# Kernel tuning notes

Hardware: AMD Instinct MI355X
Metric: run time of the kernel (lower is better)

Reference implementation:

```python
import jax, jax.numpy as jnp
import numpy as np

B, T, D, DFF, E = 4, 2048, 1024, 4096, 8


def setup_inputs() -> dict:
    key = jax.random.key(0)
    ks = jax.random.split(key, 4)
    s_in = 1.0 / np.sqrt(D)
    s_ff = 1.0 / np.sqrt(DFF)
    return {
        "x": jax.random.normal(ks[0], (B, T, D), dtype=jnp.float32),
        "gate_W": jax.random.normal(ks[1], (D, E), dtype=jnp.float32) * s_in,
        "gate_b": jnp.zeros((E,), dtype=jnp.float32),
        "W1": jax.random.normal(ks[2], (E, D, DFF), dtype=jnp.float32) * s_in,
        "b1": jnp.zeros((E, DFF), dtype=jnp.float32),
        "W2": jax.random.normal(ks[3], (E, DFF, D), dtype=jnp.float32) * s_ff,
        "b2": jnp.zeros((E, D), dtype=jnp.float32),
    }


def reference(x, gate_W, gate_b, W1, b1, W2, b2):
    # x: [B, T, D]. Top-1 gated MoE; each expert FFN runs on the (masked)
    # full token set, exactly as the original dense-masked implementation.
    b, t, d = x.shape
    num_experts = gate_W.shape[-1]
    logits = jnp.einsum("btd,de->bte", x, gate_W) + gate_b  # [B,T,E]
    top1 = jnp.argmax(logits, axis=-1).reshape(-1)          # [B*T]
    flat_x = x.reshape(b * t, d)                            # [N,D]
    out = jnp.zeros_like(flat_x)
    for e in range(num_experts):  # small fixed expert count
        mask = (top1 == e).astype(x.dtype)[:, None]         # [N,1]
        h = jax.nn.gelu((flat_x * mask) @ W1[e] + b1[e], approximate=False)
        out = out + (h @ W2[e] + b2[e]) * mask
    return out.reshape(b, t, d)
```

## Files before the change

kernel.cpp:

```cpp
#include <hip/hip_runtime.h>
#include <hip/hip_bf16.h>
#include <cstdint>

#define N_TOK 8192
#define D_IN  1024
#define DFF   4096
#define NE    8
#define DEPTH 3
#define MAXT256 40

typedef __bf16 bf16x8 __attribute__((ext_vector_type(8)));
typedef float  f32x4  __attribute__((ext_vector_type(4)));

__device__ __forceinline__ unsigned short f2bf(float f) {
  unsigned u = __float_as_uint(f);
  u += 0x7fffu + ((u >> 16) & 1u);
  return (unsigned short)(u >> 16);
}

__device__ __forceinline__ void gll16(const void* g, void* l) {
  __builtin_amdgcn_global_load_lds(
      (__attribute__((address_space(1))) void*)g,
      (__attribute__((address_space(3))) void*)l, 16, 0, 0);
}

__global__ __launch_bounds__(256) void gate_kernel(
    const float* __restrict__ x, const float* __restrict__ gW,
    const float* __restrict__ gb, unsigned short* __restrict__ xbf,
    int* __restrict__ top1) {
  int wave = threadIdx.x >> 6, lane = threadIdx.x & 63;
  int n = blockIdx.x * 4 + wave;
  const float* xr = x + (size_t)n * D_IN;
  double acc[NE];
#pragma unroll
  for (int e = 0; e < NE; ++e) acc[e] = 0.0;
#pragma unroll
  for (int j = 0; j < 16; ++j) {
    int d = j * 64 + lane;
    float v = xr[d];
    xbf[(size_t)n * D_IN + d] = f2bf(v);
    float4 g0 = *(const float4*)(gW + (size_t)d * 8);
    float4 g1 = *(const float4*)(gW + (size_t)d * 8 + 4);
    acc[0] += (double)v * (double)g0.x;
    acc[1] += (double)v * (double)g0.y;
    acc[2] += (double)v * (double)g0.z;
    acc[3] += (double)v * (double)g0.w;
    acc[4] += (double)v * (double)g1.x;
    acc[5] += (double)v * (double)g1.y;
    acc[6] += (double)v * (double)g1.z;
    acc[7] += (double)v * (double)g1.w;
  }
#pragma unroll
  for (int m = 32; m >= 1; m >>= 1) {
#pragma unroll
    for (int e = 0; e < NE; ++e) acc[e] += __shfl_xor(acc[e], m);
  }
  if (lane == 0) {
    float best = (float)acc[0] + gb[0];
    int be = 0;
#pragma unroll
    for (int e = 1; e < NE; ++e) {
      float lv = (float)acc[e] + gb[e];
      if (lv > best) { best = lv; be = e; }
    }
    top1[n] = be;
  }
}

__global__ __launch_bounds__(1024) void build_kernel(
    const int* __restrict__ top1, int* __restrict__ hdr, int* __restrict__ perm,
    int* __restrict__ tile_e, int* __restrict__ tile_m, int* __restrict__ sub0,
    int* __restrict__ t256_e, int* __restrict__ t256_m, int* __restrict__ t256_s) {
  __shared__ int cnt[NE];
  int tid = threadIdx.x;
  if (tid < NE) cnt[tid] = 0;
  __syncthreads();
  int mye[8], myp[8];
#pragma unroll
  for (int r = 0; r < 8; ++r) {
    int n = r * 1024 + tid;
    int e = top1[n];
    mye[r] = e;
    myp[r] = atomicAdd(&cnt[e], 1);
  }
  __syncthreads();
  if (tid == 0) {
    int o = 0;
    int n1 = 0, n2 = 0, n256 = 0;
    for (int e = 0; e < NE; ++e) {
      int Me = cnt[e];
      hdr[e] = Me;
      hdr[8 + e] = o;
      o += Me;
    }
    hdr[16] = o;
    for (int e = 0; e < NE; ++e) {
      int Me = cnt[e];
      int base2 = n2;
      n2 += (Me + 63) >> 6;
      for (int m0 = 0; m0 < Me; m0 += 128) {
        tile_e[n1] = e; tile_m[n1] = m0; sub0[n1] = base2 + (m0 >> 6); ++n1;
      }
      for (int m0 = 0; m0 < Me; m0 += 256) {
        t256_e[n256] = e; t256_m[n256] = m0; t256_s[n256] = base2 + (m0 >> 6); ++n256;
      }
    }
    hdr[17] = n1;
    hdr[18] = n2;
    hdr[19] = n256;
  }
  __syncthreads();
#pragma unroll
  for (int r = 0; r < 8; ++r) {
    int n = r * 1024 + tid;
    perm[mye[r] * N_TOK + myp[r]] = n;
  }
}

__global__ __launch_bounds__(256) void apack256_kernel(
    const unsigned short* __restrict__ xbf, const int* __restrict__ hdr,
    const int* __restrict__ t256_e, const int* __restrict__ t256_m,
    const int* __restrict__ perm, unsigned short* __restrict__ Apack) {
  int ti = blockIdx.x >> 3;
  if (ti >= hdr[19]) return;
  int part = blockIdx.x & 7;
  int h = part >> 2, ktq = part & 3;
  int e = t256_e[ti], m0 = t256_m[ti], Me = hdr[e];
  int w = threadIdx.x >> 6, lane = threadIdx.x & 63;
  int kq = lane >> 4, m = lane & 15;
#pragma unroll
  for (int g2 = 0; g2 < 2; ++g2) {
    int g = w * 2 + g2;
    int r = m0 + h * 128 + g * 16 + m;
    if (r >= Me) r = Me - 1;
    int token = perm[e * N_TOK + r];
    const char* src = (const char*)xbf + (size_t)token * 2048 + kq * 16;
    char* dst = (char*)Apack + (size_t)ti * 524288 + h * 8192 + g * 1024 + lane * 16;
#pragma unroll
    for (int kt2 = 0; kt2 < 8; ++kt2) {
      int kt = ktq * 8 + kt2;
      *(int4*)(dst + (size_t)kt * 16384) = *(const int4*)(src + kt * 64);
    }
  }
}

__device__ __forceinline__ void wpack_w1_body(
    const float* __restrict__ src, unsigned short* __restrict__ dst, int bid) {
  __shared__ unsigned short tile[64][72];
  int e = bid >> 10;
  int t = bid & 1023;
  int r0 = (t >> 6) * 64, c0 = (t & 63) * 64;
  const float* s = src + (size_t)e * D_IN * DFF;
  int tr = threadIdx.x >> 4, tc = (threadIdx.x & 15) * 4;
#pragma unroll
  for (int p = 0; p < 4; ++p) {
    int row = r0 + tr + p * 16;
    const float4 v = *(const float4*)(s + (size_t)row * DFF + c0 + tc);
    tile[tc + 0][tr + p * 16] = f2bf(v.x);
    tile[tc + 1][tr + p * 16] = f2bf(v.y);
    tile[tc + 2][tr + p * 16] = f2bf(v.z);
    tile[tc + 3][tr + p * 16] = f2bf(v.w);
  }
  __syncthreads();
#pragma unroll
  for (int u = 0; u < 2; ++u) {
    int c = u * 256 + threadIdx.x;
    int kk_l = c >> 8, gg_l = (c >> 6) & 3, kq = (c >> 4) & 3, mm = c & 15;
    int fl = gg_l * 16 + mm;
    int kl = kk_l * 32 + kq * 8;
    int4 val = *(const int4*)&tile[fl][kl];
    int f = c0 + fl;
    int nt = f >> 8, h = (f >> 7) & 1, g = (f >> 4) & 7;
    int kt = (r0 >> 5) + kk_l;
    size_t off = ((size_t)(e * 16 + nt) * 32 + kt) * 16384 +
                 (size_t)h * 8192 + g * 1024 + (kq * 16 + mm) * 16;
    *(int4*)((char*)dst + off) = val;
  }
}

__device__ __forceinline__ void wpack_body(
    const float* __restrict__ src, unsigned short* __restrict__ dst,
    int R, int C, int tiles_r, int tiles_c, int bid) {
  __shared__ unsigned short tile[64][72];
  int tpe = tiles_r * tiles_c;
  int e = bid / tpe;
  int t = bid % tpe;
  int r0 = (t / tiles_c) * 64, c0 = (t % tiles_c) * 64;
  const float* s = src + (size_t)e * R * C;
  int tr = threadIdx.x >> 4, tc = (threadIdx.x & 15) * 4;
#pragma unroll
  for (int p = 0; p < 4; ++p) {
    int row = r0 + tr + p * 16;
    const float4 v = *(const float4*)(s + (size_t)row * C + c0 + tc);
    tile[tc + 0][tr + p * 16] = f2bf(v.x);
    tile[tc + 1][tr + p * 16] = f2bf(v.y);
    tile[tc + 2][tr + p * 16] = f2bf(v.z);
    tile[tc + 3][tr + p * 16] = f2bf(v.w);
  }
  __syncthreads();
  int nkk = R >> 5, ntc = C >> 7;
#pragma unroll
  for (int u = 0; u < 2; ++u) {
    int c = u * 256 + threadIdx.x;
    int kk_l = c >> 8, gg_l = (c >> 6) & 3, kq = (c >> 4) & 3, mm = c & 15;
    int fl = gg_l * 16 + mm;
    int kl = kk_l * 32 + kq * 8;
    int4 val = *(const int4*)&tile[fl][kl];
    int f = c0 + fl;
    int nt = f >> 7, gg = (f >> 4) & 7;
    int kk = (r0 >> 5) + kk_l;
    size_t off = ((((size_t)e * ntc + nt) * nkk + kk) * 8 + gg) * 1024 + (kq * 16 + mm) * 16;
    *(int4*)((char*)dst + off) = val;
  }
}

__global__ __launch_bounds__(256) void wpack_both(
    const float* __restrict__ W1, unsigned short* __restrict__ B1,
    const float* __restrict__ W2, unsigned short* __restrict__ B2) {
  if (blockIdx.x < NE * 16 * 64)
    wpack_w1_body(W1, B1, blockIdx.x);
  else
    wpack_body(W2, B2, DFF, D_IN, 64, 16, blockIdx.x - NE * 16 * 64);
}

__global__ __launch_bounds__(512, 2) void gemm1_256(
    const unsigned short* __restrict__ Apack, const unsigned short* __restrict__ Bpack1,
    const float* __restrict__ b1, const int* __restrict__ hdr,
    const int* __restrict__ t256_e, const int* __restrict__ t256_m,
    const int* __restrict__ t256_s, unsigned short* __restrict__ Hpack) {
  int ti = blockIdx.x >> 4;
  if (ti >= hdr[19]) return;
  int nt = blockIdx.x & 15;
  int e = t256_e[ti], m0 = t256_m[ti], Me = hdr[e];
  int n0 = nt * 256;

  extern __shared__ __align__(16) char smem[];

  int tid = threadIdx.x, wave = tid >> 6, lane = tid & 63;
  int wm = wave >> 2, wn = wave & 3;

  const char* aBase = (const char*)Apack + (size_t)ti * 524288;
  const char* bBase = (const char*)Bpack1 + (size_t)(e * 16 + nt) * 524288;

  auto stage = [&](int kt) {
    int b = kt % 3;
    const char* sB = bBase + (size_t)kt * 16384 + tid * 16;
    char* dB = smem + 49152 + b * 16384 + tid * 16;
    gll16(sB, dB);
    gll16(sB + 8192, dB + 8192);
    const char* sA = aBase + (size_t)kt * 16384 + tid * 16;
    char* dA = smem + b * 16384 + tid * 16;
    gll16(sA, dA);
    gll16(sA + 8192, dA + 8192);
  };

  stage(0);
  stage(1);

  f32x4 acc[8][4];
#pragma unroll
  for (int i = 0; i < 8; ++i)
#pragma unroll
    for (int j = 0; j < 4; ++j) { f32x4 z = {0.f, 0.f, 0.f, 0.f}; acc[i][j] = z; }

  const int NITER = D_IN / 32;
  for (int T = 0; T < NITER; ++T) {
    asm volatile("s_waitcnt vmcnt(4)" ::: "memory");
    __builtin_amdgcn_s_barrier();
    int nx = T + 2;
    if (nx > NITER - 1) nx = NITER - 1;
    stage(nx);
    int b = T % 3;
    const char* Ap = smem + b * 16384 + wm * 8192 + lane * 16;
    const char* Bp = smem + 49152 + b * 16384 + (wn >> 1) * 8192 + (wn & 1) * 4096 + lane * 16;
    bf16x8 a[8], bf[4];
#pragma unroll
    for (int i = 0; i < 8; ++i) a[i] = *(const bf16x8*)(Ap + i * 1024);
#pragma unroll
    for (int j = 0; j < 4; ++j) bf[j] = *(const bf16x8*)(Bp + j * 1024);
#pragma unroll
    for (int i = 0; i < 8; ++i)
#pragma unroll
      for (int j = 0; j < 4; ++j)
        acc[i][j] = __builtin_amdgcn_mfma_f32_16x16x32_bf16(a[i], bf[j], acc[i][j], 0, 0, 0);
  }

  asm volatile("s_waitcnt vmcnt(0)" ::: "memory");
  __syncthreads();
  unsigned short* Cl = (unsigned short*)smem;
  int quad = lane >> 4, col_l = lane & 15;
  float bb[4];
#pragma unroll
  for (int j = 0; j < 4; ++j)
    bb[j] = b1[(size_t)e * DFF + n0 + wn * 64 + j * 16 + col_l];
  int s0 = t256_s[ti];
  int rem = Me - m0; if (rem > 256) rem = 256;
  int nsv = (rem + 63) >> 6;
#pragma unroll
  for (int h = 0; h < 2; ++h) {
    if (wm == h) {
#pragma unroll
      for (int i = 0; i < 8; ++i) {
#pragma unroll
        for (int j = 0; j < 4; ++j) {
          int lc = wn * 64 + j * 16 + col_l;
#pragma unroll
          for (int r = 0; r < 4; ++r) {
            int lr_l = i * 16 + quad * 4 + r;
            float v = acc[i][j][r] + bb[j];
            v = 0.5f * v * (1.0f + erff(v * 0.70710678118654752f));
            Cl[lr_l * 256 + lc] = f2bf(v);
          }
        }
      }
    }
    __syncthreads();
#pragma unroll
    for (int u = 0; u < 8; ++u) {
      int c = u * 512 + tid;
      int lr_l = c >> 5, fc = c & 31;
      int lr = h * 128 + lr_l;
      int sv = lr >> 6;
      if (sv < nsv) {
        int4 val = *(const int4*)(Cl + lr_l * 256 + fc * 8);
        int wi2 = s0 + sv;
        int m2 = lr & 63;
        int gg = m2 >> 4, mm = m2 & 15;
        int kk2 = nt * 8 + (fc >> 2), kq2 = fc & 3;
        *(int4*)((char*)Hpack + ((size_t)wi2 * 128 + kk2) * 4096 + gg * 1024 + (kq2 * 16 + mm) * 16) = val;
      }
    }
    __syncthreads();
  }
}

__global__ __launch_bounds__(256) void gemm2(
    const unsigned short* __restrict__ Hpack, const unsigned short* __restrict__ Bpack2,
    const float* __restrict__ b2, const int* __restrict__ hdr,
    const int* __restrict__ tile_e, const int* __restrict__ tile_m,
    const int* __restrict__ sub0, const int* __restrict__ perm,
    float* __restrict__ out) {
  int wi = blockIdx.x >> 3;
  if (wi >= hdr[17]) return;
  int nt = blockIdx.x & 7;
  int e = tile_e[wi];
  int m0 = tile_m[wi];
  int Me = hdr[e];
  int n0 = nt * 128;
  int s0 = sub0[wi];
  int s1 = (m0 + 64 < Me) ? s0 + 1 : s0;

  __shared__ __align__(16) char smem[49152];
  char* Asm = smem;
  char* Bsm = smem + 24576;

  int tid = threadIdx.x, wave = tid >> 6, lane = tid & 63;
  int wm = wave >> 1, wn = wave & 1;

  const char* abase_s[2];
  int agl[2];
  int off_s[2];
#pragma unroll
  for (int s = 0; s < 2; ++s) {
    int g = wave * 2 + s;
    int sv = g >> 2;
    abase_s[s] = (const char*)Hpack + (size_t)((sv ? s1 : s0) * 128) * 4096;
    agl[s] = (g & 3) * 1024 + lane * 16;
    off_s[s] = g * 1024 + lane * 16;
  }
  const char* bbase = (const char*)Bpack2 + (size_t)(e * 8 + nt) * 128 * 8192;

  const int NITER = DFF / 32;
#pragma unroll
  for (int p = 0; p < DEPTH; ++p) {
    gll16(abase_s[0] + (size_t)p * 4096 + agl[0], Asm + p * 8192 + off_s[0]);
    gll16(abase_s[1] + (size_t)p * 4096 + agl[1], Asm + p * 8192 + off_s[1]);
    gll16(bbase + (size_t)p * 8192 + off_s[0], Bsm + p * 8192 + off_s[0]);
    gll16(bbase + (size_t)p * 8192 + off_s[1], Bsm + p * 8192 + off_s[1]);
  }

  f32x4 acc[4][4];
#pragma unroll
  for (int i = 0; i < 4; ++i)
#pragma unroll
    for (int j = 0; j < 4; ++j) { f32x4 z = {0.f, 0.f, 0.f, 0.f}; acc[i][j] = z; }

  int cur = 0;
  for (int kk = 0; kk < NITER; ++kk) {
    asm volatile("s_waitcnt vmcnt(8)" ::: "memory");
    __builtin_amdgcn_s_barrier();
    const char* ab = Asm + cur * 8192;
    const char* bb = Bsm + cur * 8192;
    bf16x8 af[4], bfv[4];
#pragma unroll
    for (int i = 0; i < 4; ++i)
      af[i] = *(const bf16x8*)(ab + (wm * 4 + i) * 1024 + lane * 16);
#pragma unroll
    for (int j = 0; j < 4; ++j)
      bfv[j] = *(const bf16x8*)(bb + (wn * 4 + j) * 1024 + lane * 16);
    asm volatile("s_waitcnt lgkmcnt(0)" ::: "memory");
    __builtin_amdgcn_s_barrier();
    int nx = kk + DEPTH;
    if (nx > NITER - 1) nx = NITER - 1;
    char* ad = Asm + cur * 8192;
    char* bd = Bsm + cur * 8192;
    gll16(abase_s[0] + (size_t)nx * 4096 + agl[0], ad + off_s[0]);
    gll16(abase_s[1] + (size_t)nx * 4096 + agl[1], ad + off_s[1]);
    gll16(bbase + (size_t)nx * 8192 + off_s[0], bd + off_s[0]);
    gll16(bbase + (size_t)nx * 8192 + off_s[1], bd + off_s[1]);
#pragma unroll
    for (int i = 0; i < 4; ++i)
#pragma unroll
      for (int j = 0; j < 4; ++j)
        acc[i][j] = __builtin_amdgcn_mfma_f32_16x16x32_bf16(af[i], bfv[j], acc[i][j], 0, 0, 0);
    cur = (cur == DEPTH - 1) ? 0 : cur + 1;
  }

  int quad = lane >> 4, col_l = lane & 15;
#pragma unroll
  for (int i = 0; i < 4; ++i) {
    int rbase = m0 + wm * 64 + i * 16 + quad * 4;
#pragma unroll
    for (int j = 0; j < 4; ++j) {
      int col = n0 + wn * 64 + j * 16 + col_l;
      float bb = b2[(size_t)e * D_IN + col];
#pragma unroll
      for (int r = 0; r < 4; ++r) {
        int rr = rbase + r;
        if (rr < Me) {
          int token = perm[e * N_TOK + rr];
          out[(size_t)token * D_IN + col] = acc[i][j][r] + bb;
        }
      }
    }
  }
}

extern "C" void kernel_launch(void* const* d_in, const int* in_sizes, int n_in,
                              void* d_out, int out_size, void* d_ws, size_t ws_size,
                              hipStream_t stream) {
  const float* x  = (const float*)d_in[0];
  const float* gW = (const float*)d_in[1];
  const float* gb = (const float*)d_in[2];
  const float* W1 = (const float*)d_in[3];
  const float* b1 = (const float*)d_in[4];
  const float* W2 = (const float*)d_in[5];
  const float* b2 = (const float*)d_in[6];
  float* out = (float*)d_out;

  char* ws = (char*)d_ws;
  int* hdr     = (int*)ws;
  int* tile_e  = (int*)(ws + 4096);
  int* tile_m  = (int*)(ws + 4608);
  int* sub0    = (int*)(ws + 5120);
  int* t256_e  = (int*)(ws + 5632);
  int* t256_m  = (int*)(ws + 6144);
  int* t256_s  = (int*)(ws + 6656);
  int* top1    = (int*)(ws + 8192);
  int* perm    = (int*)(ws + 65536);
  unsigned short* xbf    = (unsigned short*)(ws + 524288);
  unsigned short* Bpack2 = (unsigned short*)(ws + 524288);
  unsigned short* Apack  = (unsigned short*)(ws + 69206016);
  unsigned short* Bpack1 = (unsigned short*)(ws + 92274688);
  unsigned short* Hpack  = (unsigned short*)(ws + 159383552);

  (void)hipFuncSetAttribute((const void*)gemm1_256,
                            hipFuncAttributeMaxDynamicSharedMemorySize, 98304);

  gate_kernel<<<N_TOK / 4, 256, 0, stream>>>(x, gW, gb, xbf, top1);
  build_kernel<<<1, 1024, 0, stream>>>(top1, hdr, perm, tile_e, tile_m, sub0,
                                       t256_e, t256_m, t256_s);
  apack256_kernel<<<MAXT256 * 8, 256, 0, stream>>>(xbf, hdr, t256_e, t256_m, perm, Apack);
  wpack_both<<<NE * 16 * 64 + NE * 64 * 16, 256, 0, stream>>>(W1, Bpack1, W2, Bpack2);
  gemm1_256<<<MAXT256 * 16, 512, 98304, stream>>>(Apack, Bpack1, b1, hdr,
                                                  t256_e, t256_m, t256_s, Hpack);
  gemm2<<<71 * 8, 256, 0, stream>>>(Hpack, Bpack2, b2, hdr, tile_e, tile_m, sub0, perm, out);
}
```

Before: 673.6 us.

## Deepen gemm1 LDS ring to four stages and double-buffer A fragments in registers

The gemm1 main loop moves from a 3-deep to a 4-deep LDS ring (128KB dynamic shared memory) and issues the next stage's global-to-LDS loads before the wait and barrier. A fragments for the next k-step are prefetched into a second register set while the current MFMAs run, and s_setprio raises wave priority around the MFMA block. The aim is to hide LDS read latency and global-load waits behind matrix math. It costs more registers and LDS, which may lower occupancy.

```diff
diff --git a/kernel.cpp b/kernel.cpp
--- a/kernel.cpp
+++ b/kernel.cpp
@@ -243,9 +243,9 @@
   const char* bBase = (const char*)Bpack1 + (size_t)(e * 16 + nt) * 524288;
 
   auto stage = [&](int kt) {
-    int b = kt % 3;
+    int b = kt & 3;
     const char* sB = bBase + (size_t)kt * 16384 + tid * 16;
-    char* dB = smem + 49152 + b * 16384 + tid * 16;
+    char* dB = smem + 65536 + b * 16384 + tid * 16;
     gll16(sB, dB);
     gll16(sB + 8192, dB + 8192);
     const char* sA = aBase + (size_t)kt * 16384 + tid * 16;
@@ -254,8 +254,12 @@
     gll16(sA + 8192, dA + 8192);
   };
 
+  const int NITER = D_IN / 32;
+
   stage(0);
   stage(1);
+  asm volatile("s_waitcnt vmcnt(4)" ::: "memory");
+  __builtin_amdgcn_s_barrier();
 
   f32x4 acc[8][4];
 #pragma unroll
@@ -263,26 +267,37 @@
 #pragma unroll
     for (int j = 0; j < 4; ++j) { f32x4 z = {0.f, 0.f, 0.f, 0.f}; acc[i][j] = z; }
 
-  const int NITER = D_IN / 32;
-  for (int T = 0; T < NITER; ++T) {
+  bf16x8 aA[8], aB[8], bR[4];
+  {
+    const char* Ap0 = smem + wm * 8192 + lane * 16;
+#pragma unroll
+    for (int i = 0; i < 8; ++i) aA[i] = *(const bf16x8*)(Ap0 + i * 1024);
+  }
+
+  auto iter = [&](int T, bf16x8 (&cur)[8], bf16x8 (&nxt)[8]) {
+    int nx = T + 2; if (nx > NITER - 1) nx = NITER - 1;
+    stage(nx);
     asm volatile("s_waitcnt vmcnt(4)" ::: "memory");
     __builtin_amdgcn_s_barrier();
-    int nx = T + 2;
-    if (nx > NITER - 1) nx = NITER - 1;
-    stage(nx);
-    int b = T % 3;
-    const char* Ap = smem + b * 16384 + wm * 8192 + lane * 16;
-    const char* Bp = smem + 49152 + b * 16384 + (wn >> 1) * 8192 + (wn & 1) * 4096 + lane * 16;
-    bf16x8 a[8], bf[4];
-#pragma unroll
-    for (int i = 0; i < 8; ++i) a[i] = *(const bf16x8*)(Ap + i * 1024);
-#pragma unroll
-    for (int j = 0; j < 4; ++j) bf[j] = *(const bf16x8*)(Bp + j * 1024);
+    int pT = T + 1; if (pT > NITER - 1) pT = NITER - 1;
+    const char* Bp = smem + 65536 + (T & 3) * 16384 + (wn >> 1) * 8192 + (wn & 1) * 4096 + lane * 16;
+    const char* Ap = smem + (pT & 3) * 16384 + wm * 8192 + lane * 16;
+#pragma unroll
+    for (int j = 0; j < 4; ++j) bR[j] = *(const bf16x8*)(Bp + j * 1024);
+#pragma unroll
+    for (int i = 0; i < 8; ++i) nxt[i] = *(const bf16x8*)(Ap + i * 1024);
+    __builtin_amdgcn_s_setprio(1);
 #pragma unroll
     for (int i = 0; i < 8; ++i)
 #pragma unroll
       for (int j = 0; j < 4; ++j)
-        acc[i][j] = __builtin_amdgcn_mfma_f32_16x16x32_bf16(a[i], bf[j], acc[i][j], 0, 0, 0);
+        acc[i][j] = __builtin_amdgcn_mfma_f32_16x16x32_bf16(cur[i], bR[j], acc[i][j], 0, 0, 0);
+    __builtin_amdgcn_s_setprio(0);
+  };
+
+  for (int T = 0; T < NITER; T += 2) {
+    iter(T, aA, aB);
+    iter(T + 1, aB, aA);
   }
 
   asm volatile("s_waitcnt vmcnt(0)" ::: "memory");
@@ -465,14 +480,14 @@
   unsigned short* Hpack  = (unsigned short*)(ws + 159383552);
 
   (void)hipFuncSetAttribute((const void*)gemm1_256,
-                            hipFuncAttributeMaxDynamicSharedMemorySize, 98304);
+                            hipFuncAttributeMaxDynamicSharedMemorySize, 131072);
 
   gate_kernel<<<N_TOK / 4, 256, 0, stream>>>(x, gW, gb, xbf, top1);
   build_kernel<<<1, 1024, 0, stream>>>(top1, hdr, perm, tile_e, tile_m, sub0,
                                        t256_e, t256_m, t256_s);
   apack256_kernel<<<MAXT256 * 8, 256, 0, stream>>>(xbf, hdr, t256_e, t256_m, perm, Apack);
   wpack_both<<<NE * 16 * 64 + NE * 64 * 16, 256, 0, stream>>>(W1, Bpack1, W2, Bpack2);
-  gemm1_256<<<MAXT256 * 16, 512, 98304, stream>>>(Apack, Bpack1, b1, hdr,
-                                                  t256_e, t256_m, t256_s, Hpack);
+  gemm1_256<<<MAXT256 * 16, 512, 131072, stream>>>(Apack, Bpack1, b1, hdr,
+                                                   t256_e, t256_m, t256_s, Hpack);
   gemm2<<<71 * 8, 256, 0, stream>>>(Hpack, Bpack2, b2, hdr, tile_e, tile_m, sub0, perm, out);
 }
```

Result: no change. 674.4 us (+0.1%).
